# Optimization experiments

Hardware: AMD Instinct MI355X
Metric: run time of the kernel (lower is better)

## Reference

```python
import jax, jax.numpy as jnp
import numpy as np

N, E, G = 100000, 400000, 4096
H, C = 4, 32            # heads, hidden_dim per head
D_OUT = H * C           # 128
NODE_D, EDGE_D = 38, 13
DEC_H, OUT_D = 64, 1
NEG_SLOPE = 0.2
LN_EPS = 1e-5


def setup_inputs() -> dict:
    key = jax.random.key(0)
    ks = jax.random.split(key, 40)
    r = lambda k, s: jax.random.normal(k, s, jnp.float32) * 0.1
    inp = {
        "x": jax.random.normal(ks[0], (N, NODE_D), jnp.float32),
        "edge_index": jax.random.randint(ks[1], (2, E), 0, N),
        "edge_attr": jax.random.uniform(ks[2], (E, EDGE_D), jnp.float32),
        "batch": jnp.sort(jax.random.randint(ks[3], (N,), 0, G)),
        # --- block 1 (in=38) ---
        "Wl1": r(ks[4], (NODE_D, D_OUT)), "bl1": jnp.zeros((D_OUT,), jnp.float32),
        "Wr1": r(ks[5], (NODE_D, D_OUT)), "br1": jnp.zeros((D_OUT,), jnp.float32),
        "We1": r(ks[6], (EDGE_D, D_OUT)),
        "att1": r(ks[7], (H, C)), "ab1": jnp.zeros((D_OUT,), jnp.float32),
        "ln_g1": jnp.ones((D_OUT,), jnp.float32), "ln_b1": jnp.zeros((D_OUT,), jnp.float32),
        "Wres": r(ks[8], (NODE_D, D_OUT)), "bres": jnp.zeros((D_OUT,), jnp.float32),
        # --- block 2 (in=128, residual = identity) ---
        "Wl2": r(ks[9], (D_OUT, D_OUT)), "bl2": jnp.zeros((D_OUT,), jnp.float32),
        "Wr2": r(ks[10], (D_OUT, D_OUT)), "br2": jnp.zeros((D_OUT,), jnp.float32),
        "We2": r(ks[11], (EDGE_D, D_OUT)),
        "att2": r(ks[12], (H, C)), "ab2": jnp.zeros((D_OUT,), jnp.float32),
        "ln_g2": jnp.ones((D_OUT,), jnp.float32), "ln_b2": jnp.zeros((D_OUT,), jnp.float32),
        # --- readout MLP ---
        "Wd1": r(ks[13], (D_OUT, DEC_H)), "bd1": jnp.zeros((DEC_H,), jnp.float32),
        "Wd2": r(ks[14], (DEC_H, OUT_D)), "bd2": jnp.zeros((OUT_D,), jnp.float32),
    }
    return inp


def _segment_softmax(logits, seg, n):
    m = jax.ops.segment_max(logits, seg, num_segments=n)
    ex = jnp.exp(logits - m[seg])
    s = jax.ops.segment_sum(ex, seg, num_segments=n)
    return ex / s[seg]


def _gatv2(x, src, dst, e_feat, Wl, bl, Wr, br, We, att, ab):
    n = x.shape[0]
    xl = (x @ Wl + bl).reshape(n, H, C)   # source transform
    xr = (x @ Wr + br).reshape(n, H, C)   # target transform
    ee = (e_feat @ We).reshape(-1, H, C)  # edge transform
    z = jax.nn.leaky_relu(xl[src] + xr[dst] + ee, NEG_SLOPE)  # [E,H,C]
    logits = jnp.einsum('ehc,hc->eh', z, att)                 # [E,H]
    alpha = _segment_softmax(logits, dst, n)                  # softmax over target nbhd
    out = jax.ops.segment_sum(xl[src] * alpha[..., None], dst, num_segments=n)
    return out.reshape(n, D_OUT) + ab


def _layernorm(h, g, b):
    mu = jnp.mean(h, -1, keepdims=True)
    d = h - mu
    v = jnp.mean(d * d, -1, keepdims=True)
    return d * jax.lax.rsqrt(v + LN_EPS) * g + b


def reference(x, edge_index, edge_attr, batch,
              Wl1, bl1, Wr1, br1, We1, att1, ab1, ln_g1, ln_b1, Wres, bres,
              Wl2, bl2, Wr2, br2, We2, att2, ab2, ln_g2, ln_b2,
              Wd1, bd1, Wd2, bd2):
    src, dst = edge_index[0], edge_index[1]
    n = x.shape[0]
    # add_self_loops(fill_value='mean'): self-loop edge attr = mean of incoming edge attrs
    deg = jax.ops.segment_sum(jnp.ones((src.shape[0],), x.dtype), dst, num_segments=n)
    loop_attr = jax.ops.segment_sum(edge_attr, dst, num_segments=n) / jnp.clip(deg, 1.0)[:, None]
    nodes = jnp.arange(n)
    src_a = jnp.concatenate([src, nodes])
    dst_a = jnp.concatenate([dst, nodes])
    ea = jnp.concatenate([edge_attr, loop_attr], axis=0)

    # block 1
    h = _gatv2(x, src_a, dst_a, ea, Wl1, bl1, Wr1, br1, We1, att1, ab1)
    h = jax.nn.elu(h)
    h = _layernorm(h + (x @ Wres + bres), ln_g1, ln_b1)
    # block 2 (identity residual)
    h2 = _gatv2(h, src_a, dst_a, ea, Wl2, bl2, Wr2, br2, We2, att2, ab2)
    h2 = jax.nn.elu(h2)
    h2 = _layernorm(h2 + h, ln_g2, ln_b2)

    # global mean pool over graphs
    cnt = jax.ops.segment_sum(jnp.ones((n,), x.dtype), batch, num_segments=G)
    g = jax.ops.segment_sum(h2, batch, num_segments=G) / jnp.clip(cnt, 1.0)[:, None]

    return jax.nn.relu(g @ Wd1 + bd1) @ Wd2 + bd2
```

## Files before the change

kernel.cpp:

```cpp
#include <hip/hip_runtime.h>

typedef unsigned short u16;
typedef unsigned int   u32;
typedef __attribute__((ext_vector_type(8))) short short8;
typedef __attribute__((ext_vector_type(4))) float float4v;
typedef __attribute__((ext_vector_type(2))) float float2v;

#define NODE_D   38
#define EDGE_D   13
#define D_OUT    128
#define NEG_SLOPE 0.2f
#define LN_EPS   1e-5f

__device__ __forceinline__ float bf2f(u16 v) { return __uint_as_float(((u32)v) << 16); }
__device__ __forceinline__ u16 f2bf(float f) {
    u32 u = __float_as_uint(f);
    u += 0x7fffu + ((u >> 16) & 1u);
    return (u16)(u >> 16);
}

__global__ void k_pre(const int* __restrict__ dst, int E, int* __restrict__ deg,
                      const int* __restrict__ batch, int N, int G, int* __restrict__ goff) {
    int i = blockIdx.x * blockDim.x + threadIdx.x;
    if (i < E) atomicAdd(deg + dst[i], 1);
    if (i < N) {
        int b = batch[i];
        int prev = (i == 0) ? -1 : batch[i - 1];
        for (int g = prev + 1; g <= b; g++) goff[g] = i;
        if (i == N - 1)
            for (int g = b + 1; g <= G; g++) goff[g] = N;
    }
}

#define SCAN_CHUNK 1024
__global__ void k_scan1(const int* __restrict__ cnt, int N, int addone, int* __restrict__ bsum) {
    __shared__ int sh[256];
    int base = blockIdx.x * SCAN_CHUNK;
    int t = threadIdx.x;
    int s = 0;
#pragma unroll
    for (int i = 0; i < 4; i++) { int idx = base + t * 4 + i; if (idx < N) s += cnt[idx] + addone; }
    sh[t] = s; __syncthreads();
    for (int ofs = 128; ofs > 0; ofs >>= 1) {
        if (t < ofs) sh[t] += sh[t + ofs];
        __syncthreads();
    }
    if (t == 0) bsum[blockIdx.x] = sh[0];
}
__global__ void k_scan2(const int* __restrict__ bsum, int nb, int* __restrict__ boff) {
    __shared__ int sh[256];
    int t = threadIdx.x;
    if (nb <= 256) {
        int v = (t < nb) ? bsum[t] : 0;
        sh[t] = v; __syncthreads();
        for (int ofs = 1; ofs < 256; ofs <<= 1) {
            int x = (t >= ofs) ? sh[t - ofs] : 0;
            __syncthreads();
            sh[t] += x;
            __syncthreads();
        }
        if (t < nb) boff[t] = sh[t] - v;
        if (t == nb - 1) boff[nb] = sh[t];
    } else if (t == 0) {
        int run = 0;
        for (int i = 0; i < nb; i++) { boff[i] = run; run += bsum[i]; }
        boff[nb] = run;
    }
}
__global__ void k_scan3(const int* __restrict__ cnt, int N, int addone,
                        const int* __restrict__ boff, int nb, int* __restrict__ off) {
    __shared__ int wtot[4];
    int base = blockIdx.x * SCAN_CHUNK;
    int t = threadIdx.x;
    int lane = t & 63, w = t >> 6;
    int v[4]; int s = 0;
#pragma unroll
    for (int i = 0; i < 4; i++) { int idx = base + t * 4 + i; v[i] = (idx < N) ? cnt[idx] + addone : 0; s += v[i]; }
    int inc = s;
#pragma unroll
    for (int ofs = 1; ofs < 64; ofs <<= 1) {
        int x = __shfl_up(inc, ofs, 64);
        if (lane >= ofs) inc += x;
    }
    if (lane == 63) wtot[w] = inc;
    __syncthreads();
    int wofs = 0;
    for (int i = 0; i < w; i++) wofs += wtot[i];
    int run = boff[blockIdx.x] + wofs + (inc - s);
#pragma unroll
    for (int i = 0; i < 4; i++) {
        int idx = base + t * 4 + i;
        if (idx < N) off[idx] = run;
        run += v[i];
    }
    if (blockIdx.x == 0 && t == 0) off[N] = boff[nb];
}

__global__ void k_fill(const int* __restrict__ src, const int* __restrict__ dst,
                       const float* __restrict__ eattr, int E,
                       const int* __restrict__ csr_off, int* __restrict__ fill,
                       int* __restrict__ csr_src, u16* __restrict__ A) {
    int e = blockIdx.x * blockDim.x + threadIdx.x;
    if (e >= E) return;
    int d = dst[e];
    int pos = csr_off[d] + atomicAdd(fill + d, 1);
    csr_src[pos] = src[e];
    u16 row[16];
#pragma unroll
    for (int k = 0; k < EDGE_D; k++) row[k] = f2bf(eattr[(size_t)e * EDGE_D + k]);
#pragma unroll
    for (int k = EDGE_D; k < 16; k++) row[k] = 0;
    uint4* rp = (uint4*)(A + (size_t)pos * 16);
    rp[0] = (uint4){(u32)row[0] | ((u32)row[1] << 16), (u32)row[2] | ((u32)row[3] << 16),
                    (u32)row[4] | ((u32)row[5] << 16), (u32)row[6] | ((u32)row[7] << 16)};
    rp[1] = (uint4){(u32)row[8] | ((u32)row[9] << 16), (u32)row[10] | ((u32)row[11] << 16),
                    (u32)row[12] | ((u32)row[13] << 16), (u32)row[14] | ((u32)row[15] << 16)};
}

__global__ void k_self(const int* __restrict__ csr_off, int N,
                       int* __restrict__ csr_src, u16* __restrict__ A) {
    int tid = blockIdx.x * blockDim.x + threadIdx.x;
    if (tid >= N * 16) return;
    int n = tid >> 4, k = tid & 15;
    int b = csr_off[n], e2 = csr_off[n + 1] - 1;
    u16 v = 0;
    if (k < EDGE_D) {
        float s = 0.f;
        for (int j = b; j < e2; j++) s += bf2f(A[(size_t)j * 16 + k]);
        v = f2bf(s / fmaxf((float)(e2 - b), 1.f));
    }
    A[(size_t)e2 * 16 + k] = v;
    if (k == 0) csr_src[e2] = n;
}

template <int KPAD, int CT, int KREAL, bool IN_BF16>
__global__ __launch_bounds__(256) void k_tf_mfma(
    const void* __restrict__ in_v,
    const float* __restrict__ W0, const float* __restrict__ b0,
    const float* __restrict__ W1, const float* __restrict__ b1,
    const float* __restrict__ W2, const float* __restrict__ b2,
    u16* __restrict__ o0, u16* __restrict__ o1, u16* __restrict__ o2,
    int N) {
    constexpr int RS = KPAD + 8;
    __shared__ u16 Bsw[CT * 16 * RS];
    __shared__ float bsh[CT * 16];
    const float* Ws[3] = {W0, W1, W2};
    const float* bs[3] = {b0, b1, b2};
    u16* outs[3] = {o0, o1, o2};
    int t = threadIdx.x;
    for (int i = t; i < CT * 16 * KPAD; i += 256) {
        int c = i / KPAD, k = i - c * KPAD;
        float v = (k < KREAL) ? Ws[c >> 7][(size_t)k * 128 + (c & 127)] : 0.f;
        Bsw[c * RS + k] = f2bf(v);
    }
    for (int i = t; i < CT * 16; i += 256) bsh[i] = bs[i >> 7][i & 127];
    __syncthreads();

    int wid = t >> 6, lane = t & 63;
    int quad = lane >> 4, m = lane & 15;

    for (int g0 = blockIdx.x * 64; g0 < N; g0 += gridDim.x * 64) {
        int na = g0 + wid * 16 + m;
        if (na > N - 1) na = N - 1;
        short8 a[KPAD / 32];
        if (IN_BF16) {
            const u16* in = (const u16*)in_v;
#pragma unroll
            for (int kc = 0; kc < KPAD / 32; kc++)
                a[kc] = *(const short8*)(in + (size_t)na * KPAD + kc * 32 + quad * 8);
        } else {
            const float* in = (const float*)in_v;
#pragma unroll
            for (int kc = 0; kc < KPAD / 32; kc++)
#pragma unroll
                for (int j = 0; j < 8; j++) {
                    int k = kc * 32 + quad * 8 + j;
                    float v = (k < KREAL) ? in[(size_t)na * KREAL + k] : 0.f;
                    a[kc][j] = (short)f2bf(v);
                }
        }
        float4v acc[CT];
#pragma unroll
        for (int ct = 0; ct < CT; ct++) acc[ct] = (float4v){0.f, 0.f, 0.f, 0.f};
#pragma unroll
        for (int ct = 0; ct < CT; ct++) {
#pragma unroll
            for (int kc = 0; kc < KPAD / 32; kc++) {
                short8 b = *(const short8*)(&Bsw[(ct * 16 + m) * RS + kc * 32 + quad * 8]);
                acc[ct] = __builtin_amdgcn_mfma_f32_16x16x32_bf16(a[kc], b, acc[ct], 0, 0, 0);
            }
        }
#pragma unroll
        for (int ct = 0; ct < CT; ct++) {
            int col = ct * 16 + m;
            u16* op = outs[col >> 7];
            int cc = col & 127;
            float bv = bsh[col];
#pragma unroll
            for (int r = 0; r < 4; r++) {
                int node = g0 + wid * 16 + quad * 4 + r;
                if (node < N) op[(size_t)node * 128 + cc] = f2bf(acc[ct][r] + bv);
            }
        }
    }
}

__global__ __launch_bounds__(256) void k_gat(
    const int* __restrict__ csr_off, const int* __restrict__ csr_src,
    const u16* __restrict__ A_csr,
    const u16* __restrict__ xl, const u16* __restrict__ xr,
    const u16* __restrict__ res, const float* __restrict__ We,
    const float* __restrict__ att, const float* __restrict__ ab,
    const float* __restrict__ lng, const float* __restrict__ lnb,
    u16* __restrict__ hout, int N, int npw) {
    int t = threadIdx.x;
    int wid = t >> 6, lane = t & 63;
    int wave = blockIdx.x * 4 + wid;
    int n0 = wave * npw;
    if (n0 >= N) return;
    int n1 = n0 + npw; if (n1 > N) n1 = N;

    float2v we2[EDGE_D];
#pragma unroll
    for (int k = 0; k < EDGE_D; k++)
        we2[k] = (float2v){We[k * D_OUT + 2 * lane], We[k * D_OUT + 2 * lane + 1]};
    float a0 = att[2 * lane], a1 = att[2 * lane + 1];
    float abv0 = ab[2 * lane], abv1 = ab[2 * lane + 1];
    float lg0 = lng[2 * lane], lg1 = lng[2 * lane + 1];
    float lb0 = lnb[2 * lane], lb1 = lnb[2 * lane + 1];

    const u32* xl32 = (const u32*)xl;
    int wbeg = csr_off[n0];
    int wend = csr_off[n1];
    int cl = wend - 1;

    u32 xw = xl32[(size_t)csr_src[wbeg] * 64 + lane];
    const uint4* ap = (const uint4*)(A_csr + (size_t)wbeg * 16);
    uint4 aq0 = ap[0], aq1 = ap[1];

    int i = wbeg;
    for (int n = n0; n < n1; n++) {
        int end = csr_off[n + 1];
        u32 xrw = ((const u32*)xr)[(size_t)n * 64 + lane];
        float2v xr2 = (float2v){bf2f((u16)(xrw & 0xffff)), bf2f((u16)(xrw >> 16))};

        float ssum = 0.f;
        float2v acc2 = (float2v){0.f, 0.f};
        for (; i < end; i++) {
            u32 xwc = xw;
            uint4 q0 = aq0, q1 = aq1;
            {
                int ip = (i + 1 < wend) ? i + 1 : cl;
                xw = xl32[(size_t)csr_src[ip] * 64 + lane];
                const uint4* ap2 = (const uint4*)(A_csr + (size_t)ip * 16);
                aq0 = ap2[0]; aq1 = ap2[1];
            }
            u32 dw[8] = {q0.x, q0.y, q0.z, q0.w, q1.x, q1.y, q1.z, q1.w};
            float2v ee = (float2v){0.f, 0.f};
#pragma unroll
            for (int k = 0; k < EDGE_D; k++) {
                u32 d = dw[k >> 1];
                float av = bf2f((u16)((k & 1) ? (d >> 16) : (d & 0xffff)));
                ee += we2[k] * av;
            }
            float2v xs = (float2v){bf2f((u16)(xwc & 0xffff)), bf2f((u16)(xwc >> 16))};
            float2v z = xs + xr2 + ee;
            float z0 = z[0], z1 = z[1];
            z0 = (z0 > 0.f) ? z0 : z0 * NEG_SLOPE;
            z1 = (z1 > 0.f) ? z1 : z1 * NEG_SLOPE;
            float p = z0 * a0 + z1 * a1;
            p += __shfl_xor(p, 1, 64);
            p += __shfl_xor(p, 2, 64);
            p += __shfl_xor(p, 4, 64);
            p += __shfl_xor(p, 8, 64);
            float wgt = __expf(p);
            ssum += wgt;
            acc2 += xs * wgt;
        }

        float inv = 1.f / ssum;
        float o0 = acc2[0] * inv + abv0;
        float o1 = acc2[1] * inv + abv1;
        o0 = (o0 > 0.f) ? o0 : (__expf(o0) - 1.f);
        o1 = (o1 > 0.f) ? o1 : (__expf(o1) - 1.f);
        u32 rw = ((const u32*)res)[(size_t)n * 64 + lane];
        o0 += bf2f((u16)(rw & 0xffff));
        o1 += bf2f((u16)(rw >> 16));
        float sm = o0 + o1;
#pragma unroll
        for (int mk = 1; mk < 64; mk <<= 1) sm += __shfl_xor(sm, mk, 64);
        float mu = sm * (1.f / 128.f);
        float d0 = o0 - mu, d1 = o1 - mu;
        float vv = d0 * d0 + d1 * d1;
#pragma unroll
        for (int mk = 1; mk < 64; mk <<= 1) vv += __shfl_xor(vv, mk, 64);
        float rs = rsqrtf(vv * (1.f / 128.f) + LN_EPS);
        float h0 = d0 * rs * lg0 + lb0;
        float h1 = d1 * rs * lg1 + lb1;
        ((u32*)hout)[(size_t)n * 64 + lane] = (u32)f2bf(h0) | ((u32)f2bf(h1) << 16);
    }
}

__global__ __launch_bounds__(128) void k_pool_read(
    const u16* __restrict__ h2, const int* __restrict__ goff,
    const float* __restrict__ Wd1, const float* __restrict__ bd1,
    const float* __restrict__ Wd2, const float* __restrict__ bd2,
    float* __restrict__ out, int G) {
    __shared__ float psh[128];
    __shared__ float rsh[2][64];
    int g = blockIdx.x;
    int c = threadIdx.x;
    int b = goff[g], e = goff[g + 1];
    float s = 0.f;
    for (int n = b; n < e; n++) s += bf2f(h2[(size_t)n * 128 + c]);
    psh[c] = s / fmaxf((float)(e - b), 1.f);
    __syncthreads();
    int j = c & 63, hw = c >> 6;
    float acc = (hw == 0) ? bd1[j] : 0.f;
    int k0 = hw * 64;
    for (int k = k0; k < k0 + 64; k++)
        acc += psh[k] * Wd1[k * 64 + j];
    rsh[hw][j] = acc;
    __syncthreads();
    if (c < 64) {
        float a = fmaxf(rsh[0][c] + rsh[1][c], 0.f);
        float v = a * Wd2[c];
#pragma unroll
        for (int mk = 1; mk < 64; mk <<= 1) v += __shfl_xor(v, mk, 64);
        if (c == 0) out[g] = v + bd2[0];
    }
}

extern "C" void kernel_launch(void* const* d_in, const int* in_sizes, int n_in,
                              void* d_out, int out_size, void* d_ws, size_t ws_size,
                              hipStream_t stream) {
    const float* x     = (const float*)d_in[0];
    const int*   eidx  = (const int*)d_in[1];
    const float* eattr = (const float*)d_in[2];
    const int*   batch = (const int*)d_in[3];
    const float* Wl1 = (const float*)d_in[4],  *bl1 = (const float*)d_in[5];
    const float* Wr1 = (const float*)d_in[6],  *br1 = (const float*)d_in[7];
    const float* We1 = (const float*)d_in[8],  *att1 = (const float*)d_in[9],  *ab1 = (const float*)d_in[10];
    const float* lng1 = (const float*)d_in[11], *lnb1 = (const float*)d_in[12];
    const float* Wres = (const float*)d_in[13], *bres = (const float*)d_in[14];
    const float* Wl2 = (const float*)d_in[15], *bl2 = (const float*)d_in[16];
    const float* Wr2 = (const float*)d_in[17], *br2 = (const float*)d_in[18];
    const float* We2 = (const float*)d_in[19], *att2 = (const float*)d_in[20], *ab2 = (const float*)d_in[21];
    const float* lng2 = (const float*)d_in[22], *lnb2 = (const float*)d_in[23];
    const float* Wd1 = (const float*)d_in[24], *bd1 = (const float*)d_in[25];
    const float* Wd2 = (const float*)d_in[26], *bd2 = (const float*)d_in[27];

    int N = in_sizes[0] / NODE_D;
    int E = in_sizes[1] / 2;
    int G = out_size;
    int EN = E + N;
    const int* src = eidx;
    const int* dst = eidx + E;

    char* w = (char*)d_ws;
    auto alloc = [&](size_t bytes) -> char* {
        char* p = w;
        w += (bytes + 255) & ~(size_t)255;
        return p;
    };
    int NB = (N + SCAN_CHUNK - 1) / SCAN_CHUNK;
    int*   csr_off  = (int*)alloc((size_t)(N + 1) * 4);
    int*   csr_src  = (int*)alloc((size_t)EN * 4);
    u16*   A_csr    = (u16*)alloc((size_t)(EN + 64) * 16 * 2);
    u16*   xlb      = (u16*)alloc((size_t)N * D_OUT * 2);
    u16*   xrb      = (u16*)alloc((size_t)N * D_OUT * 2);
    u16*   resb     = (u16*)alloc((size_t)N * D_OUT * 2);
    u16*   hb       = (u16*)alloc((size_t)N * D_OUT * 2);
    int*   goff     = (int*)alloc((size_t)(G + 1) * 4);
    size_t szN = ((size_t)N * 4 + 255) & ~(size_t)255;
    char*  zp   = alloc(2 * szN);
    int*   deg  = (int*)zp;
    int*   fill = (int*)(zp + szN);
    int*   bsum = (int*)alloc((size_t)(NB + 1) * 4);
    int*   boff = (int*)alloc((size_t)(NB + 1) * 4);

    hipMemsetAsync(zp, 0, 2 * szN, stream);

    int mx = (E > N) ? E : N;
    k_pre<<<(mx + 255) / 256, 256, 0, stream>>>(dst, E, deg, batch, N, G, goff);

    k_scan1<<<NB, 256, 0, stream>>>(deg, N, 1, bsum);
    k_scan2<<<1, 256, 0, stream>>>(bsum, NB, boff);
    k_scan3<<<NB, 256, 0, stream>>>(deg, N, 1, boff, NB, csr_off);
    k_fill<<<(E + 255) / 256, 256, 0, stream>>>(src, dst, eattr, E, csr_off, fill, csr_src, A_csr);
    k_self<<<((size_t)N * 16 + 255) / 256, 256, 0, stream>>>(csr_off, N, csr_src, A_csr);

    int npw = 4;
    int gblocks = (N + npw * 4 - 1) / (npw * 4);

    k_tf_mfma<64, 24, NODE_D, false><<<640, 256, 0, stream>>>(
        x, Wl1, bl1, Wr1, br1, Wres, bres, xlb, xrb, resb, N);
    k_gat<<<gblocks, 256, 0, stream>>>(csr_off, csr_src, A_csr,
                                       xlb, xrb, resb, We1, att1, ab1, lng1, lnb1, hb, N, npw);

    k_tf_mfma<128, 16, 128, true><<<640, 256, 0, stream>>>(
        hb, Wl2, bl2, Wr2, br2, Wr2, br2, xlb, xrb, xrb, N);
    k_gat<<<gblocks, 256, 0, stream>>>(csr_off, csr_src, A_csr,
                                       xlb, xrb, hb, We2, att2, ab2, lng2, lnb2, resb, N, npw);

    k_pool_read<<<G, 128, 0, stream>>>(resb, goff, Wd1, bd1, Wd2, bd2, (float*)d_out, G);
}
```

Measured before the change: 578.0 us.

## Pad CSR rows to even length and process two edges per iteration in GAT

Each node's CSR segment is padded to an even length with a masked dummy edge, which lets the GAT kernel handle two edges per iteration with deeper prefetch. Source indices are gathered once per wave and then broadcast by shuffle. Cross-lane reductions switch to DPP for the 16-lane stages, and bf16 unpacking is done with bit masks. The node features are cast to bf16 in a separate kernel so the first transform can read bf16 input. The cost is more padding traffic, an extra kernel launch, and a fallback path for waves that own more than 64 edges.

```diff
diff --git a/kernel.cpp b/kernel.cpp
--- a/kernel.cpp
+++ b/kernel.cpp
@@ -17,6 +17,25 @@
     u32 u = __float_as_uint(f);
     u += 0x7fffu + ((u >> 16) & 1u);
     return (u16)(u >> 16);
+}
+
+template <int CTRL>
+__device__ __forceinline__ float dpp_radd(float x) {
+    int t = __builtin_amdgcn_update_dpp(0, __float_as_int(x), CTRL, 0xf, 0xf, true);
+    return x + __int_as_float(t);
+}
+__device__ __forceinline__ float reduce16(float p) {
+    p = dpp_radd<0xB1>(p);
+    p = dpp_radd<0x4E>(p);
+    p = dpp_radd<0x124>(p);
+    p = dpp_radd<0x128>(p);
+    return p;
+}
+__device__ __forceinline__ float reduce64(float v) {
+    v = reduce16(v);
+    v += __shfl_xor(v, 16, 64);
+    v += __shfl_xor(v, 32, 64);
+    return v;
 }
 
 __global__ void k_pre(const int* __restrict__ dst, int E, int* __restrict__ deg,
@@ -32,14 +51,25 @@
     }
 }
 
+__global__ void k_xcast(const float* __restrict__ x, u16* __restrict__ xb, int N) {
+    int i = blockIdx.x * blockDim.x + threadIdx.x;
+    if (i >= N * 32) return;
+    int n = i >> 5, kk = (i & 31) * 2;
+    float f0 = (kk < NODE_D) ? x[(size_t)n * NODE_D + kk] : 0.f;
+    float f1 = (kk + 1 < NODE_D) ? x[(size_t)n * NODE_D + kk + 1] : 0.f;
+    ((u32*)xb)[(size_t)n * 32 + (i & 31)] = (u32)f2bf(f0) | ((u32)f2bf(f1) << 16);
+}
+
 #define SCAN_CHUNK 1024
-__global__ void k_scan1(const int* __restrict__ cnt, int N, int addone, int* __restrict__ bsum) {
+__device__ __forceinline__ int padcnt(int d) { return (d + 2) & ~1; }
+
+__global__ void k_scan1(const int* __restrict__ cnt, int N, int* __restrict__ bsum) {
     __shared__ int sh[256];
     int base = blockIdx.x * SCAN_CHUNK;
     int t = threadIdx.x;
     int s = 0;
 #pragma unroll
-    for (int i = 0; i < 4; i++) { int idx = base + t * 4 + i; if (idx < N) s += cnt[idx] + addone; }
+    for (int i = 0; i < 4; i++) { int idx = base + t * 4 + i; if (idx < N) s += padcnt(cnt[idx]); }
     sh[t] = s; __syncthreads();
     for (int ofs = 128; ofs > 0; ofs >>= 1) {
         if (t < ofs) sh[t] += sh[t + ofs];
@@ -67,7 +97,7 @@
         boff[nb] = run;
     }
 }
-__global__ void k_scan3(const int* __restrict__ cnt, int N, int addone,
+__global__ void k_scan3(const int* __restrict__ cnt, int N,
                         const int* __restrict__ boff, int nb, int* __restrict__ off) {
     __shared__ int wtot[4];
     int base = blockIdx.x * SCAN_CHUNK;
@@ -75,7 +105,7 @@
     int lane = t & 63, w = t >> 6;
     int v[4]; int s = 0;
 #pragma unroll
-    for (int i = 0; i < 4; i++) { int idx = base + t * 4 + i; v[i] = (idx < N) ? cnt[idx] + addone : 0; s += v[i]; }
+    for (int i = 0; i < 4; i++) { int idx = base + t * 4 + i; v[i] = (idx < N) ? padcnt(cnt[idx]) : 0; s += v[i]; }
     int inc = s;
 #pragma unroll
     for (int ofs = 1; ofs < 64; ofs <<= 1) {
@@ -117,20 +147,27 @@
                     (u32)row[12] | ((u32)row[13] << 16), (u32)row[14] | ((u32)row[15] << 16)};
 }
 
-__global__ void k_self(const int* __restrict__ csr_off, int N,
+__global__ void k_self(const int* __restrict__ csr_off, const int* __restrict__ deg, int N,
                        int* __restrict__ csr_src, u16* __restrict__ A) {
     int tid = blockIdx.x * blockDim.x + threadIdx.x;
     if (tid >= N * 16) return;
     int n = tid >> 4, k = tid & 15;
-    int b = csr_off[n], e2 = csr_off[n + 1] - 1;
+    int b = csr_off[n];
+    int d = deg[n];
+    int self = b + d;
     u16 v = 0;
     if (k < EDGE_D) {
         float s = 0.f;
-        for (int j = b; j < e2; j++) s += bf2f(A[(size_t)j * 16 + k]);
-        v = f2bf(s / fmaxf((float)(e2 - b), 1.f));
-    }
-    A[(size_t)e2 * 16 + k] = v;
-    if (k == 0) csr_src[e2] = n;
+        for (int j = b; j < self; j++) s += bf2f(A[(size_t)j * 16 + k]);
+        v = f2bf(s / fmaxf((float)d, 1.f));
+    }
+    A[(size_t)self * 16 + k] = v;
+    if (k == 0) csr_src[self] = n;
+    int e = csr_off[n + 1];
+    if (self + 1 < e) {
+        A[(size_t)(self + 1) * 16 + k] = 0;
+        if (k == 0) csr_src[self + 1] = n | (int)0x80000000;
+    }
 }
 
 template <int KPAD, int CT, int KREAL, bool IN_BF16>
@@ -230,54 +267,12 @@
     float lb0 = lnb[2 * lane], lb1 = lnb[2 * lane + 1];
 
     const u32* xl32 = (const u32*)xl;
+    const u32* xr32 = (const u32*)xr;
     int wbeg = csr_off[n0];
     int wend = csr_off[n1];
-    int cl = wend - 1;
-
-    u32 xw = xl32[(size_t)csr_src[wbeg] * 64 + lane];
-    const uint4* ap = (const uint4*)(A_csr + (size_t)wbeg * 16);
-    uint4 aq0 = ap[0], aq1 = ap[1];
-
-    int i = wbeg;
-    for (int n = n0; n < n1; n++) {
-        int end = csr_off[n + 1];
-        u32 xrw = ((const u32*)xr)[(size_t)n * 64 + lane];
-        float2v xr2 = (float2v){bf2f((u16)(xrw & 0xffff)), bf2f((u16)(xrw >> 16))};
-
-        float ssum = 0.f;
-        float2v acc2 = (float2v){0.f, 0.f};
-        for (; i < end; i++) {
-            u32 xwc = xw;
-            uint4 q0 = aq0, q1 = aq1;
-            {
-                int ip = (i + 1 < wend) ? i + 1 : cl;
-                xw = xl32[(size_t)csr_src[ip] * 64 + lane];
-                const uint4* ap2 = (const uint4*)(A_csr + (size_t)ip * 16);
-                aq0 = ap2[0]; aq1 = ap2[1];
-            }
-            u32 dw[8] = {q0.x, q0.y, q0.z, q0.w, q1.x, q1.y, q1.z, q1.w};
-            float2v ee = (float2v){0.f, 0.f};
-#pragma unroll
-            for (int k = 0; k < EDGE_D; k++) {
-                u32 d = dw[k >> 1];
-                float av = bf2f((u16)((k & 1) ? (d >> 16) : (d & 0xffff)));
-                ee += we2[k] * av;
-            }
-            float2v xs = (float2v){bf2f((u16)(xwc & 0xffff)), bf2f((u16)(xwc >> 16))};
-            float2v z = xs + xr2 + ee;
-            float z0 = z[0], z1 = z[1];
-            z0 = (z0 > 0.f) ? z0 : z0 * NEG_SLOPE;
-            z1 = (z1 > 0.f) ? z1 : z1 * NEG_SLOPE;
-            float p = z0 * a0 + z1 * a1;
-            p += __shfl_xor(p, 1, 64);
-            p += __shfl_xor(p, 2, 64);
-            p += __shfl_xor(p, 4, 64);
-            p += __shfl_xor(p, 8, 64);
-            float wgt = __expf(p);
-            ssum += wgt;
-            acc2 += xs * wgt;
-        }
-
+    int nedge = wend - wbeg;
+
+    auto finish = [&](int n, float ssum, float2v acc2) {
         float inv = 1.f / ssum;
         float o0 = acc2[0] * inv + abv0;
         float o1 = acc2[1] * inv + abv1;
@@ -286,18 +281,124 @@
         u32 rw = ((const u32*)res)[(size_t)n * 64 + lane];
         o0 += bf2f((u16)(rw & 0xffff));
         o1 += bf2f((u16)(rw >> 16));
-        float sm = o0 + o1;
-#pragma unroll
-        for (int mk = 1; mk < 64; mk <<= 1) sm += __shfl_xor(sm, mk, 64);
+        float sm = reduce64(o0 + o1);
         float mu = sm * (1.f / 128.f);
         float d0 = o0 - mu, d1 = o1 - mu;
-        float vv = d0 * d0 + d1 * d1;
-#pragma unroll
-        for (int mk = 1; mk < 64; mk <<= 1) vv += __shfl_xor(vv, mk, 64);
+        float vv = reduce64(d0 * d0 + d1 * d1);
         float rs = rsqrtf(vv * (1.f / 128.f) + LN_EPS);
         float h0 = d0 * rs * lg0 + lb0;
         float h1 = d1 * rs * lg1 + lb1;
         ((u32*)hout)[(size_t)n * 64 + lane] = (u32)f2bf(h0) | ((u32)f2bf(h1) << 16);
+    };
+
+    const float2v z0v = (float2v){0.f, 0.f};
+
+    if (nedge <= 64) {
+        int last = nedge - 1;
+        int sv = csr_src[wbeg + min(lane, last)];
+        int sA = __shfl(sv, 0, 64);
+        int sB = __shfl(sv, min(1, last), 64);
+        int sC = __shfl(sv, min(2, last), 64);
+        int sD = __shfl(sv, min(3, last), 64);
+        u32 xwA = xl32[(size_t)(sA & 0x7fffffff) * 64 + lane];
+        u32 xwB = xl32[(size_t)(sB & 0x7fffffff) * 64 + lane];
+        const uint4* apA = (const uint4*)(A_csr + (size_t)wbeg * 16);
+        const uint4* apB = (const uint4*)(A_csr + (size_t)(wbeg + min(1, last)) * 16);
+        uint4 aqA0 = apA[0], aqA1 = apA[1];
+        uint4 aqB0 = apB[0], aqB1 = apB[1];
+
+        int i = wbeg;
+        for (int n = n0; n < n1; n++) {
+            int end = csr_off[n + 1];
+            u32 xrw = xr32[(size_t)n * 64 + lane];
+            float2v xr2 = (float2v){bf2f((u16)(xrw & 0xffff)), bf2f((u16)(xrw >> 16))};
+            float ssum = 0.f;
+            float2v acc2 = (float2v){0.f, 0.f};
+            for (; i < end; i += 2) {
+                u32 xwC = xl32[(size_t)(sC & 0x7fffffff) * 64 + lane];
+                u32 xwD = xl32[(size_t)(sD & 0x7fffffff) * 64 + lane];
+                int jC = i + 2 - wbeg; if (jC > last) jC = last;
+                int jD = i + 3 - wbeg; if (jD > last) jD = last;
+                const uint4* apC = (const uint4*)(A_csr + (size_t)(wbeg + jC) * 16);
+                const uint4* apD = (const uint4*)(A_csr + (size_t)(wbeg + jD) * 16);
+                uint4 aqC0 = apC[0], aqC1 = apC[1];
+                uint4 aqD0 = apD[0], aqD1 = apD[1];
+                int jE = i + 4 - wbeg; if (jE > last) jE = last;
+                int jF = i + 5 - wbeg; if (jF > last) jF = last;
+                int sE = __shfl(sv, jE, 64);
+                int sF = __shfl(sv, jF, 64);
+
+                u32 dwA[8] = {aqA0.x, aqA0.y, aqA0.z, aqA0.w, aqA1.x, aqA1.y, aqA1.z, aqA1.w};
+                u32 dwB[8] = {aqB0.x, aqB0.y, aqB0.z, aqB0.w, aqB1.x, aqB1.y, aqB1.z, aqB1.w};
+                float2v eeA = (float2v){0.f, 0.f}, eeB = (float2v){0.f, 0.f};
+#pragma unroll
+                for (int k = 0; k < EDGE_D; k++) {
+                    u32 da = dwA[k >> 1], db = dwB[k >> 1];
+                    float ava = __uint_as_float((k & 1) ? (da & 0xffff0000u) : (da << 16));
+                    float avb = __uint_as_float((k & 1) ? (db & 0xffff0000u) : (db << 16));
+                    eeA += we2[k] * ava;
+                    eeB += we2[k] * avb;
+                }
+                float2v xsA = (float2v){bf2f((u16)(xwA & 0xffff)), bf2f((u16)(xwA >> 16))};
+                float2v xsB = (float2v){bf2f((u16)(xwB & 0xffff)), bf2f((u16)(xwB >> 16))};
+                float2v zA = xsA + xr2 + eeA;
+                float2v zB = xsB + xr2 + eeB;
+                float2v lA = __builtin_elementwise_max(zA, z0v) + __builtin_elementwise_min(zA, z0v) * NEG_SLOPE;
+                float2v lB = __builtin_elementwise_max(zB, z0v) + __builtin_elementwise_min(zB, z0v) * NEG_SLOPE;
+                float pA = lA[0] * a0 + lA[1] * a1;
+                float pB = lB[0] * a0 + lB[1] * a1;
+                pA = reduce16(pA);
+                pB = reduce16(pB);
+                float wA = (sA < 0) ? 0.f : __expf(pA);
+                float wB = (sB < 0) ? 0.f : __expf(pB);
+                ssum += wA + wB;
+                acc2 += xsA * wA;
+                acc2 += xsB * wB;
+                xwA = xwC; xwB = xwD;
+                aqA0 = aqC0; aqA1 = aqC1; aqB0 = aqD0; aqB1 = aqD1;
+                sA = sC; sB = sD; sC = sE; sD = sF;
+            }
+            finish(n, ssum, acc2);
+        }
+    } else {
+        int cl = wend - 1;
+        int f = csr_src[wbeg];
+        u32 xw = xl32[(size_t)(f & 0x7fffffff) * 64 + lane];
+        const uint4* ap = (const uint4*)(A_csr + (size_t)wbeg * 16);
+        uint4 aq0 = ap[0], aq1 = ap[1];
+        int i = wbeg;
+        for (int n = n0; n < n1; n++) {
+            int end = csr_off[n + 1];
+            u32 xrw = xr32[(size_t)n * 64 + lane];
+            float2v xr2 = (float2v){bf2f((u16)(xrw & 0xffff)), bf2f((u16)(xrw >> 16))};
+            float ssum = 0.f;
+            float2v acc2 = (float2v){0.f, 0.f};
+            for (; i < end; i++) {
+                u32 xwc = xw; uint4 q0 = aq0, q1 = aq1; int fc = f;
+                int ip = (i + 1 < wend) ? i + 1 : cl;
+                f = csr_src[ip];
+                xw = xl32[(size_t)(f & 0x7fffffff) * 64 + lane];
+                const uint4* ap2 = (const uint4*)(A_csr + (size_t)ip * 16);
+                aq0 = ap2[0]; aq1 = ap2[1];
+                u32 dw[8] = {q0.x, q0.y, q0.z, q0.w, q1.x, q1.y, q1.z, q1.w};
+                float2v ee = (float2v){0.f, 0.f};
+#pragma unroll
+                for (int k = 0; k < EDGE_D; k++) {
+                    u32 d = dw[k >> 1];
+                    float av = __uint_as_float((k & 1) ? (d & 0xffff0000u) : (d << 16));
+                    ee += we2[k] * av;
+                }
+                float2v xs = (float2v){bf2f((u16)(xwc & 0xffff)), bf2f((u16)(xwc >> 16))};
+                float2v z = xs + xr2 + ee;
+                float2v lz = __builtin_elementwise_max(z, z0v) + __builtin_elementwise_min(z, z0v) * NEG_SLOPE;
+                float p = lz[0] * a0 + lz[1] * a1;
+                p = reduce16(p);
+                float wgt = (fc < 0) ? 0.f : __expf(p);
+                ssum += wgt;
+                acc2 += xs * wgt;
+            }
+            finish(n, ssum, acc2);
+        }
     }
 }
 
@@ -353,7 +454,7 @@
     int N = in_sizes[0] / NODE_D;
     int E = in_sizes[1] / 2;
     int G = out_size;
-    int EN = E + N;
+    int ENp = E + 2 * N;
     const int* src = eidx;
     const int* dst = eidx + E;
 
@@ -365,8 +466,9 @@
     };
     int NB = (N + SCAN_CHUNK - 1) / SCAN_CHUNK;
     int*   csr_off  = (int*)alloc((size_t)(N + 1) * 4);
-    int*   csr_src  = (int*)alloc((size_t)EN * 4);
-    u16*   A_csr    = (u16*)alloc((size_t)(EN + 64) * 16 * 2);
+    int*   csr_src  = (int*)alloc((size_t)ENp * 4);
+    u16*   A_csr    = (u16*)alloc((size_t)(ENp + 64) * 16 * 2);
+    u16*   xb       = (u16*)alloc((size_t)N * 64 * 2);
     u16*   xlb      = (u16*)alloc((size_t)N * D_OUT * 2);
     u16*   xrb      = (u16*)alloc((size_t)N * D_OUT * 2);
     u16*   resb     = (u16*)alloc((size_t)N * D_OUT * 2);
@@ -384,17 +486,19 @@
     int mx = (E > N) ? E : N;
     k_pre<<<(mx + 255) / 256, 256, 0, stream>>>(dst, E, deg, batch, N, G, goff);
 
-    k_scan1<<<NB, 256, 0, stream>>>(deg, N, 1, bsum);
+    k_xcast<<<(N * 32 + 255) / 256, 256, 0, stream>>>(x, xb, N);
+
+    k_scan1<<<NB, 256, 0, stream>>>(deg, N, bsum);
     k_scan2<<<1, 256, 0, stream>>>(bsum, NB, boff);
-    k_scan3<<<NB, 256, 0, stream>>>(deg, N, 1, boff, NB, csr_off);
+    k_scan3<<<NB, 256, 0, stream>>>(deg, N, boff, NB, csr_off);
     k_fill<<<(E + 255) / 256, 256, 0, stream>>>(src, dst, eattr, E, csr_off, fill, csr_src, A_csr);
-    k_self<<<((size_t)N * 16 + 255) / 256, 256, 0, stream>>>(csr_off, N, csr_src, A_csr);
+    k_self<<<((size_t)N * 16 + 255) / 256, 256, 0, stream>>>(csr_off, deg, N, csr_src, A_csr);
 
     int npw = 4;
     int gblocks = (N + npw * 4 - 1) / (npw * 4);
 
-    k_tf_mfma<64, 24, NODE_D, false><<<640, 256, 0, stream>>>(
-        x, Wl1, bl1, Wr1, br1, Wres, bres, xlb, xrb, resb, N);
+    k_tf_mfma<64, 24, NODE_D, true><<<640, 256, 0, stream>>>(
+        xb, Wl1, bl1, Wr1, br1, Wres, bres, xlb, xrb, resb, N);
     k_gat<<<gblocks, 256, 0, stream>>>(csr_off, csr_src, A_csr,
                                        xlb, xrb, resb, We1, att1, ab1, lng1, lnb1, hb, N, npw);
 
```

Result: slower. 624.4 us (+8.0%).

## Deepen GAT edge prefetch, use DPP reductions, pre-convert x to bf16

Applied to the files above, without the earlier changes.

In the GAT aggregation kernel, a wave whose edge range fits in 64 loads all its source indices at once with one coalesced read and uses readlane to prefetch source features two edges ahead. This removes the dependent index load from the critical path. Cross-lane reductions now use DPP row operations instead of ds_swizzle/shuffle, and leaky-relu uses max/min. The input x is converted to padded bf16 inside the preprocessing kernel so the first transform can take the bf16 MFMA path. That adds a large thread grid (N*32) to k_pre.

```diff
diff --git a/kernel.cpp b/kernel.cpp
--- a/kernel.cpp
+++ b/kernel.cpp
@@ -19,8 +19,28 @@
     return (u16)(u >> 16);
 }
 
+template <int CTRL>
+__device__ __forceinline__ float dpp_radd(float x) {
+    int t = __builtin_amdgcn_update_dpp(0, __float_as_int(x), CTRL, 0xf, 0xf, true);
+    return x + __int_as_float(t);
+}
+__device__ __forceinline__ float reduce16(float p) {
+    p = dpp_radd<0xB1>(p);
+    p = dpp_radd<0x4E>(p);
+    p = dpp_radd<0x124>(p);
+    p = dpp_radd<0x128>(p);
+    return p;
+}
+__device__ __forceinline__ float reduce64(float v) {
+    v = reduce16(v);
+    v += __shfl_xor(v, 16, 64);
+    v += __shfl_xor(v, 32, 64);
+    return v;
+}
+
 __global__ void k_pre(const int* __restrict__ dst, int E, int* __restrict__ deg,
-                      const int* __restrict__ batch, int N, int G, int* __restrict__ goff) {
+                      const int* __restrict__ batch, int N, int G, int* __restrict__ goff,
+                      const float* __restrict__ x, u16* __restrict__ xb) {
     int i = blockIdx.x * blockDim.x + threadIdx.x;
     if (i < E) atomicAdd(deg + dst[i], 1);
     if (i < N) {
@@ -29,6 +49,12 @@
         for (int g = prev + 1; g <= b; g++) goff[g] = i;
         if (i == N - 1)
             for (int g = b + 1; g <= G; g++) goff[g] = N;
+    }
+    if (i < N * 32) {
+        int n = i >> 5, kk = (i & 31) * 2;
+        float f0 = (kk < NODE_D) ? x[(size_t)n * NODE_D + kk] : 0.f;
+        float f1 = (kk + 1 < NODE_D) ? x[(size_t)n * NODE_D + kk + 1] : 0.f;
+        ((u32*)xb)[(size_t)n * 32 + (i & 31)] = (u32)f2bf(f0) | ((u32)f2bf(f1) << 16);
     }
 }
 
@@ -230,54 +256,12 @@
     float lb0 = lnb[2 * lane], lb1 = lnb[2 * lane + 1];
 
     const u32* xl32 = (const u32*)xl;
+    const u32* xr32 = (const u32*)xr;
     int wbeg = csr_off[n0];
     int wend = csr_off[n1];
-    int cl = wend - 1;
-
-    u32 xw = xl32[(size_t)csr_src[wbeg] * 64 + lane];
-    const uint4* ap = (const uint4*)(A_csr + (size_t)wbeg * 16);
-    uint4 aq0 = ap[0], aq1 = ap[1];
-
-    int i = wbeg;
-    for (int n = n0; n < n1; n++) {
-        int end = csr_off[n + 1];
-        u32 xrw = ((const u32*)xr)[(size_t)n * 64 + lane];
-        float2v xr2 = (float2v){bf2f((u16)(xrw & 0xffff)), bf2f((u16)(xrw >> 16))};
-
-        float ssum = 0.f;
-        float2v acc2 = (float2v){0.f, 0.f};
-        for (; i < end; i++) {
-            u32 xwc = xw;
-            uint4 q0 = aq0, q1 = aq1;
-            {
-                int ip = (i + 1 < wend) ? i + 1 : cl;
-                xw = xl32[(size_t)csr_src[ip] * 64 + lane];
-                const uint4* ap2 = (const uint4*)(A_csr + (size_t)ip * 16);
-                aq0 = ap2[0]; aq1 = ap2[1];
-            }
-            u32 dw[8] = {q0.x, q0.y, q0.z, q0.w, q1.x, q1.y, q1.z, q1.w};
-            float2v ee = (float2v){0.f, 0.f};
-#pragma unroll
-            for (int k = 0; k < EDGE_D; k++) {
-                u32 d = dw[k >> 1];
-                float av = bf2f((u16)((k & 1) ? (d >> 16) : (d & 0xffff)));
-                ee += we2[k] * av;
-            }
-            float2v xs = (float2v){bf2f((u16)(xwc & 0xffff)), bf2f((u16)(xwc >> 16))};
-            float2v z = xs + xr2 + ee;
-            float z0 = z[0], z1 = z[1];
-            z0 = (z0 > 0.f) ? z0 : z0 * NEG_SLOPE;
-            z1 = (z1 > 0.f) ? z1 : z1 * NEG_SLOPE;
-            float p = z0 * a0 + z1 * a1;
-            p += __shfl_xor(p, 1, 64);
-            p += __shfl_xor(p, 2, 64);
-            p += __shfl_xor(p, 4, 64);
-            p += __shfl_xor(p, 8, 64);
-            float wgt = __expf(p);
-            ssum += wgt;
-            acc2 += xs * wgt;
-        }
-
+    int nedge = wend - wbeg;
+
+    auto finish = [&](int n, float ssum, float2v acc2) {
         float inv = 1.f / ssum;
         float o0 = acc2[0] * inv + abv0;
         float o1 = acc2[1] * inv + abv1;
@@ -286,18 +270,105 @@
         u32 rw = ((const u32*)res)[(size_t)n * 64 + lane];
         o0 += bf2f((u16)(rw & 0xffff));
         o1 += bf2f((u16)(rw >> 16));
-        float sm = o0 + o1;
-#pragma unroll
-        for (int mk = 1; mk < 64; mk <<= 1) sm += __shfl_xor(sm, mk, 64);
+        float sm = reduce64(o0 + o1);
         float mu = sm * (1.f / 128.f);
         float d0 = o0 - mu, d1 = o1 - mu;
-        float vv = d0 * d0 + d1 * d1;
-#pragma unroll
-        for (int mk = 1; mk < 64; mk <<= 1) vv += __shfl_xor(vv, mk, 64);
+        float vv = reduce64(d0 * d0 + d1 * d1);
         float rs = rsqrtf(vv * (1.f / 128.f) + LN_EPS);
         float h0 = d0 * rs * lg0 + lb0;
         float h1 = d1 * rs * lg1 + lb1;
         ((u32*)hout)[(size_t)n * 64 + lane] = (u32)f2bf(h0) | ((u32)f2bf(h1) << 16);
+    };
+
+    const float2v z0v = (float2v){0.f, 0.f};
+
+    if (nedge <= 64) {
+        int last = nedge - 1;
+        int sv = csr_src[wbeg + ((lane < nedge) ? lane : last)];
+        int f0 = __builtin_amdgcn_readlane(sv, 0);
+        int f1 = __builtin_amdgcn_readlane(sv, (1 <= last) ? 1 : last);
+        u32 xw0 = xl32[(size_t)f0 * 64 + lane];
+        u32 xw1 = xl32[(size_t)f1 * 64 + lane];
+        const uint4* ap = (const uint4*)(A_csr + (size_t)wbeg * 16);
+        uint4 aq0 = ap[0], aq1 = ap[1];
+
+        int i = wbeg;
+        for (int n = n0; n < n1; n++) {
+            int end = csr_off[n + 1];
+            u32 xrw = xr32[(size_t)n * 64 + lane];
+            float2v xr2 = (float2v){bf2f((u16)(xrw & 0xffff)), bf2f((u16)(xrw >> 16))};
+            float ssum = 0.f;
+            float2v acc2 = (float2v){0.f, 0.f};
+            for (; i < end; i++) {
+                int j2 = i + 2 - wbeg; if (j2 > last) j2 = last;
+                int f2 = __builtin_amdgcn_readlane(sv, j2);
+                u32 xwN = xl32[(size_t)f2 * 64 + lane];
+                int j1n = i + 1 - wbeg; if (j1n > last) j1n = last;
+                const uint4* apn = (const uint4*)(A_csr + (size_t)(wbeg + j1n) * 16);
+                uint4 an0 = apn[0], an1 = apn[1];
+
+                u32 dw[8] = {aq0.x, aq0.y, aq0.z, aq0.w, aq1.x, aq1.y, aq1.z, aq1.w};
+                float2v eeA = (float2v){0.f, 0.f}, eeB = (float2v){0.f, 0.f};
+#pragma unroll
+                for (int k = 0; k < EDGE_D; k++) {
+                    u32 d = dw[k >> 1];
+                    float av = __uint_as_float((k & 1) ? (d & 0xffff0000u) : (d << 16));
+                    if ((k >> 1) & 1) eeB += we2[k] * av;
+                    else             eeA += we2[k] * av;
+                }
+                float2v xs = (float2v){bf2f((u16)(xw0 & 0xffff)), bf2f((u16)(xw0 >> 16))};
+                float2v z = (xs + xr2) + (eeA + eeB);
+                float2v lz = __builtin_elementwise_max(z, z0v) + __builtin_elementwise_min(z, z0v) * NEG_SLOPE;
+                float p = lz[0] * a0 + lz[1] * a1;
+                p = reduce16(p);
+                float wgt = __expf(p);
+                ssum += wgt;
+                acc2 += xs * wgt;
+                xw0 = xw1; xw1 = xwN;
+                aq0 = an0; aq1 = an1;
+            }
+            finish(n, ssum, acc2);
+        }
+    } else {
+        int cl = wend - 1;
+        int f = csr_src[wbeg];
+        u32 xw = xl32[(size_t)f * 64 + lane];
+        const uint4* ap = (const uint4*)(A_csr + (size_t)wbeg * 16);
+        uint4 aq0 = ap[0], aq1 = ap[1];
+        int i = wbeg;
+        for (int n = n0; n < n1; n++) {
+            int end = csr_off[n + 1];
+            u32 xrw = xr32[(size_t)n * 64 + lane];
+            float2v xr2 = (float2v){bf2f((u16)(xrw & 0xffff)), bf2f((u16)(xrw >> 16))};
+            float ssum = 0.f;
+            float2v acc2 = (float2v){0.f, 0.f};
+            for (; i < end; i++) {
+                u32 xwc = xw; uint4 q0 = aq0, q1 = aq1;
+                int ip = (i + 1 < wend) ? i + 1 : cl;
+                f = csr_src[ip];
+                xw = xl32[(size_t)f * 64 + lane];
+                const uint4* ap2 = (const uint4*)(A_csr + (size_t)ip * 16);
+                aq0 = ap2[0]; aq1 = ap2[1];
+                u32 dw[8] = {q0.x, q0.y, q0.z, q0.w, q1.x, q1.y, q1.z, q1.w};
+                float2v eeA = (float2v){0.f, 0.f}, eeB = (float2v){0.f, 0.f};
+#pragma unroll
+                for (int k = 0; k < EDGE_D; k++) {
+                    u32 d = dw[k >> 1];
+                    float av = __uint_as_float((k & 1) ? (d & 0xffff0000u) : (d << 16));
+                    if ((k >> 1) & 1) eeB += we2[k] * av;
+                    else             eeA += we2[k] * av;
+                }
+                float2v xs = (float2v){bf2f((u16)(xwc & 0xffff)), bf2f((u16)(xwc >> 16))};
+                float2v z = (xs + xr2) + (eeA + eeB);
+                float2v lz = __builtin_elementwise_max(z, z0v) + __builtin_elementwise_min(z, z0v) * NEG_SLOPE;
+                float p = lz[0] * a0 + lz[1] * a1;
+                p = reduce16(p);
+                float wgt = __expf(p);
+                ssum += wgt;
+                acc2 += xs * wgt;
+            }
+            finish(n, ssum, acc2);
+        }
     }
 }
 
@@ -367,6 +438,7 @@
     int*   csr_off  = (int*)alloc((size_t)(N + 1) * 4);
     int*   csr_src  = (int*)alloc((size_t)EN * 4);
     u16*   A_csr    = (u16*)alloc((size_t)(EN + 64) * 16 * 2);
+    u16*   xb       = (u16*)alloc((size_t)N * 64 * 2);
     u16*   xlb      = (u16*)alloc((size_t)N * D_OUT * 2);
     u16*   xrb      = (u16*)alloc((size_t)N * D_OUT * 2);
     u16*   resb     = (u16*)alloc((size_t)N * D_OUT * 2);
@@ -381,8 +453,8 @@
 
     hipMemsetAsync(zp, 0, 2 * szN, stream);
 
-    int mx = (E > N) ? E : N;
-    k_pre<<<(mx + 255) / 256, 256, 0, stream>>>(dst, E, deg, batch, N, G, goff);
+    int mx = (E > N * 32) ? E : N * 32;
+    k_pre<<<(mx + 255) / 256, 256, 0, stream>>>(dst, E, deg, batch, N, G, goff, x, xb);
 
     k_scan1<<<NB, 256, 0, stream>>>(deg, N, 1, bsum);
     k_scan2<<<1, 256, 0, stream>>>(bsum, NB, boff);
@@ -393,8 +465,8 @@
     int npw = 4;
     int gblocks = (N + npw * 4 - 1) / (npw * 4);
 
-    k_tf_mfma<64, 24, NODE_D, false><<<640, 256, 0, stream>>>(
-        x, Wl1, bl1, Wr1, br1, Wres, bres, xlb, xrb, resb, N);
+    k_tf_mfma<64, 24, NODE_D, true><<<640, 256, 0, stream>>>(
+        xb, Wl1, bl1, Wr1, br1, Wres, bres, xlb, xrb, resb, N);
     k_gat<<<gblocks, 256, 0, stream>>>(csr_off, csr_src, A_csr,
                                        xlb, xrb, resb, We1, att1, ab1, lng1, lnb1, hb, N, npw);
 
```

Result: no change. 588.6 us (+1.8%).
